# Performance work log

Measured on AMD Instinct MI355X. Metric: run time of the kernel, lower is better.

Reference implementation:

```python
import jax, jax.numpy as jnp
import numpy as np

B, T_PREV, T_CUR = 256, 128, 129
N_COV, N_TREAT, N_CONF = 30, 57, 5
H, FC = 128, 128
D_IN = N_COV + N_TREAT            # 87, lstm external input size
D_CELL = D_IN + N_CONF            # 92, cell input = [x_t, z_{t-1}]


def setup_inputs() -> dict:
    key = jax.random.key(0)
    ks = jax.random.split(key, 18)
    s = 0.05
    return {
        "previous_covariates": jax.random.normal(ks[0], (B, T_PREV, N_COV), jnp.float32),
        "previous_treatments": jax.random.normal(ks[1], (B, T_PREV, N_TREAT), jnp.float32),
        "current_covariates": jax.random.normal(ks[2], (B, T_CUR, N_COV), jnp.float32),
        "init_input": jax.random.normal(ks[3], (1, 1, D_IN), jnp.float32) * s,
        "h0": jax.random.normal(ks[4], (1, H), jnp.float32) * s,
        "c0": jax.random.normal(ks[5], (1, H), jnp.float32) * s,
        "z0": jax.random.normal(ks[6], (1, N_CONF), jnp.float32) * s,
        "W_ih": jax.random.normal(ks[7], (4 * H, D_CELL), jnp.float32) * s,
        "W_hh": jax.random.normal(ks[8], (4 * H, H), jnp.float32) * s,
        "b_ih": jax.random.normal(ks[9], (4 * H,), jnp.float32) * s,
        "b_hh": jax.random.normal(ks[10], (4 * H,), jnp.float32) * s,
        "W_z": jax.random.normal(ks[11], (N_CONF, H), jnp.float32) * s,
        "b_z": jax.random.normal(ks[12], (N_CONF,), jnp.float32) * s,
        "dec_W1": jax.random.normal(ks[13], (N_TREAT, N_COV + N_CONF, FC), jnp.float32) * s,
        "dec_b1": jax.random.normal(ks[14], (N_TREAT, FC), jnp.float32) * s,
        "dec_W2": jax.random.normal(ks[15], (N_TREAT, FC), jnp.float32) * s,
        "dec_b2": jax.random.normal(ks[16], (N_TREAT,), jnp.float32) * s,
    }


def _forward(previous_covariates, previous_treatments, current_covariates,
             init_input, h0, c0, z0, W_ih, W_hh, b_ih, b_hh, W_z, b_z,
             dec_W1, dec_b1, dec_W2, dec_b2):
    Bn = previous_covariates.shape[0]
    # (T_PREV, B, D_IN)
    x = jnp.concatenate([previous_covariates, previous_treatments], -1).transpose(1, 0, 2)
    # prepend trainable init input -> (T_CUR, B, D_IN)
    rnn_in = jnp.concatenate([jnp.broadcast_to(init_input, (1, Bn, D_IN)), x], 0)

    bias = b_ih + b_hh

    def step(carry, xt):
        h, c, z = carry
        inp = jnp.concatenate([xt, z], -1)                 # (B, D_CELL)
        gates = inp @ W_ih.T + h @ W_hh.T + bias           # (B, 4H)
        i, f, g, o = jnp.split(gates, 4, axis=-1)          # torch LSTMCell gate order
        c = jax.nn.sigmoid(f) * c + jax.nn.sigmoid(i) * jnp.tanh(g)
        h = jax.nn.sigmoid(o) * jnp.tanh(c)
        z = h @ W_z.T + b_z                                # (B, N_CONF)
        return (h, c, z), z

    carry0 = (jnp.broadcast_to(h0, (Bn, H)),
              jnp.broadcast_to(c0, (Bn, H)),
              jnp.broadcast_to(z0, (Bn, N_CONF)))
    _, zs = jax.lax.scan(step, carry0, rnn_in)             # (T_CUR, B, N_CONF)

    hidden_confounders = zs.reshape(-1, N_CONF)            # (T_CUR*B, N_CONF)
    covariates = current_covariates.transpose(1, 0, 2).reshape(-1, N_COV)
    # shapes match by construction (T_CUR*B rows each) -> no pad branch
    multitask_input = jnp.concatenate([hidden_confounders, covariates], -1)  # (N, 35)

    # batched per-treatment Linear -> LeakyReLU(0.01) -> Linear
    hdec = jax.nn.leaky_relu(
        jnp.einsum('nc,tcf->ntf', multitask_input, dec_W1) + dec_b1, 0.01)
    preds = jnp.einsum('ntf,tf->nt', hdec, dec_W2) + dec_b2                   # (N, 57)

    # T_CUR*B % (T_PREV) == 0 with these shapes -> no element trim
    confounders = hidden_confounders.reshape(T_PREV, -1, N_CONF)              # (128, 258, 5)
    return preds, confounders


def reference(previous_covariates, previous_treatments, current_covariates,
              init_input, h0, c0, z0, W_ih, W_hh, b_ih, b_hh, W_z, b_z,
              dec_W1, dec_b1, dec_W2, dec_b2):
    return _forward(previous_covariates, previous_treatments, current_covariates,
                    init_input, h0, c0, z0, W_ih, W_hh, b_ih, b_hh, W_z, b_z,
                    dec_W1, dec_b1, dec_W2, dec_b2)
```

## Files before the change

### kernel.cpp

```cpp
#include <hip/hip_runtime.h>
#include <stdint.h>

#define BATCH 256
#define T_PREVN 128
#define T_CURN 129
#define N_COV 30
#define N_TREAT 57
#define N_CONF 5
#define HID 128
#define D_IN 87
#define D_CELL 92
#define GATES 512
#define PRED_N (T_CURN*BATCH)
#define CONF_OFF (PRED_N*N_TREAT)

#define OFF_W1   0
#define SZ_W1    (57*8*2*64*8*2)
#define OFF_WIH  SZ_W1
#define SZ_WIH   (32*3*64*8*2)
#define OFF_GX   (OFF_W1 + SZ_W1 + SZ_WIH)
#define SZ_GX    (PRED_N*512*2)
#define OFF_MT   (OFF_GX + SZ_GX)
#define SZ_MT    (PRED_N*40*2)
#define WS_GX    (OFF_MT + SZ_MT)
#define WS_NEED  SZ_W1
#define WS_NEED2 (SZ_W1 + SZ_MT)

typedef _Float16 h2 __attribute__((ext_vector_type(2)));
typedef _Float16 h4 __attribute__((ext_vector_type(4)));
typedef _Float16 h8 __attribute__((ext_vector_type(8)));
typedef float f32x4 __attribute__((ext_vector_type(4)));

__device__ inline float rcp_fast(float x){
#if __has_builtin(__builtin_amdgcn_rcpf)
    return __builtin_amdgcn_rcpf(x);
#else
    return 1.0f / x;
#endif
}
__device__ inline float sigmoid_f(float x){ return rcp_fast(1.0f + __expf(-x)); }
__device__ inline float tanh_f(float x){ return 1.0f - 2.0f*rcp_fast(1.0f + __expf(2.0f*x)); }

__device__ inline float dot2f(h2 a, h2 b, float c){
#if __has_builtin(__builtin_amdgcn_fdot2)
    return __builtin_amdgcn_fdot2(a, b, c, false);
#else
    return c + (float)a.x*(float)b.x + (float)a.y*(float)b.y;
#endif
}
__device__ inline unsigned short f2us(float v){
    _Float16 h = (_Float16)v;
    return __builtin_bit_cast(unsigned short, h);
}
__device__ inline h2 us2h2(unsigned int u){
    return __builtin_bit_cast(h2, u);
}

__global__ __launch_bounds__(256) void prepack_wih(const float* __restrict__ W_ih,
                                                   _Float16* __restrict__ wihf)
{
    const int tid = blockIdx.x*256 + threadIdx.x;
    const int ct  = tid / 192;
    const int rem = tid - ct*192;
    const int ks  = rem >> 6;
    const int l   = rem & 63;
    const int gate = ct*16 + (l & 15);
    const int kb   = ks*32 + ((l >> 4) << 3);
    h8 v;
    #pragma unroll
    for (int j = 0; j < 8; j++){
        const int k = kb + j;
        v[j] = (k < D_IN) ? (_Float16)W_ih[gate*D_CELL + k] : (_Float16)0.0f;
    }
    *(h8*)(wihf + (size_t)tid*8) = v;
}

__global__ __launch_bounds__(256, 2) void gx_gemm(
    const float* __restrict__ pc, const float* __restrict__ pt,
    const float* __restrict__ init_input,
    const _Float16* __restrict__ wihf, _Float16* __restrict__ Gx)
{
    __shared__ alignas(16) _Float16 a_lds[64*104];
    __shared__ alignas(16) _Float16 gx_lds[64*264];

    const int tid = threadIdx.x;
    const int nb  = blockIdx.x * 64;

    for (int idx = tid; idx < 64*96; idx += 256){
        const int r = idx / 96;
        const int k = idx - r*96;
        const int n = nb + r;
        const int bb = n / 129;
        const int t  = n - bb*129;
        float v = 0.0f;
        if (k < D_IN){
            if (t == 0) v = init_input[k];
            else        v = (k < N_COV) ? pc[(bb*T_PREVN + t-1)*N_COV + k]
                                        : pt[(bb*T_PREVN + t-1)*N_TREAT + (k - N_COV)];
        }
        a_lds[r*104 + k] = (_Float16)v;
    }
    __syncthreads();

    const int w    = tid >> 6;
    const int l    = tid & 63;
    const int col  = l & 15;
    const int quad = l >> 4;

    const _Float16* ar = a_lds + (w*16 + col)*104 + quad*8;
    const h8 a0 = *(const h8*)(ar);
    const h8 a1 = *(const h8*)(ar + 32);
    const h8 a2 = *(const h8*)(ar + 64);

    for (int half = 0; half < 2; half++){
        #pragma unroll
        for (int ct8 = 0; ct8 < 16; ct8++){
            const int ct = half*16 + ct8;
            const _Float16* bp = wihf + (size_t)ct*1536 + l*8;
            const h8 b0 = *(const h8*)(bp);
            const h8 b1 = *(const h8*)(bp + 512);
            const h8 b2 = *(const h8*)(bp + 1024);
            f32x4 acc = {0.f, 0.f, 0.f, 0.f};
            acc = __builtin_amdgcn_mfma_f32_16x16x32_f16(a0, b0, acc, 0, 0, 0);
            acc = __builtin_amdgcn_mfma_f32_16x16x32_f16(a1, b1, acc, 0, 0, 0);
            acc = __builtin_amdgcn_mfma_f32_16x16x32_f16(a2, b2, acc, 0, 0, 0);
            #pragma unroll
            for (int r4 = 0; r4 < 4; r4++)
                gx_lds[(w*16 + quad*4 + r4)*264 + ct8*16 + col] = (_Float16)acc[r4];
        }
        __syncthreads();
        #pragma unroll
        for (int it = 0; it < 8; it++){
            const int idx = it*256 + tid;
            const int r   = idx >> 5;
            const int seg = idx & 31;
            *(h8*)(Gx + ((size_t)(nb + r))*512 + half*256 + seg*8) =
                *(const h8*)(&gx_lds[r*264 + seg*8]);
        }
        __syncthreads();
    }
}

__global__ __launch_bounds__(1024, 4) void lstm_scan_gx(
    const float* __restrict__ h0, const float* __restrict__ c0,
    const float* __restrict__ z0,
    const float* __restrict__ W_ih, const float* __restrict__ W_hh,
    const float* __restrict__ b_ih, const float* __restrict__ b_hh,
    const float* __restrict__ W_z, const float* __restrict__ b_z,
    const _Float16* __restrict__ Gx,
    float* __restrict__ zs_out, _Float16* __restrict__ mT)
{
    const int b   = blockIdx.x;
    const int tid = threadIdx.x;
    const int grp = tid >> 2;
    const int j   = tid & 3;
    const int g0  = grp*2, g1 = g0 + 1;

    __shared__ alignas(16) unsigned short v16h[128];
    __shared__ alignas(16) unsigned short hall[T_CURN*136];
    __shared__ alignas(16) float gbuf[GATES];
    __shared__ alignas(16) unsigned short gxc[2][16*512];
    __shared__ alignas(16) _Float16 wz16[5*HID];
    __shared__ alignas(16) float wzf[5*HID];
    __shared__ float z0c[5];

    for (int i = tid; i < 5*HID; i += 1024) wzf[i] = W_z[i];

    float c = 0.0f;
    if (tid < HID){ v16h[tid] = f2us(h0[tid]); c = c0[tid]; }

    if (tid < 5){
        float acc0 = 0.0f, acc1 = 0.0f;
        #pragma unroll 8
        for (int u = 0; u < HID; u += 2){
            acc0 += W_z[tid*HID + u]     * h0[u];
            acc1 += W_z[tid*HID + u + 1] * h0[u + 1];
        }
        z0c[tid] = z0[tid] - b_z[tid] - (acc0 + acc1);
    }
    {
        const int row = tid >> 6;
        const uint4 q = *(const uint4*)(Gx + ((size_t)b*T_CURN + row)*512 + (size_t)(tid & 63)*8);
        *(uint4*)(&gxc[0][tid*8]) = q;
    }
    __syncthreads();

    float wz0[5], wz1[5];
    #pragma unroll
    for (int z = 0; z < 5; z++){
        wz0[z] = W_ih[g0*D_CELL + D_IN + z];
        wz1[z] = W_ih[g1*D_CELL + D_IN + z];
    }
    float be0 = b_ih[g0] + b_hh[g0];
    float be1 = b_ih[g1] + b_hh[g1];
    #pragma unroll
    for (int z = 0; z < 5; z++){ be0 += wz0[z]*b_z[z]; be1 += wz1[z]*b_z[z]; }

    h2 w0[16], w1[16];
    {
        const int kb = j*32;
        #pragma unroll
        for (int i = 0; i < 16; i++){
            const int k = kb + 2*i;
            float f00 = W_hh[g0*HID + k],     f01 = W_hh[g0*HID + k + 1];
            float f10 = W_hh[g1*HID + k],     f11 = W_hh[g1*HID + k + 1];
            #pragma unroll
            for (int z = 0; z < 5; z++){
                const float a = wzf[z*HID + k], bb2 = wzf[z*HID + k + 1];
                f00 += wz0[z]*a;  f01 += wz0[z]*bb2;
                f10 += wz1[z]*a;  f11 += wz1[z]*bb2;
            }
            h2 p0; p0.x = (_Float16)f00; p0.y = (_Float16)f01; w0[i] = p0;
            h2 p1; p1.x = (_Float16)f10; p1.y = (_Float16)f11; w1[i] = p1;
        }
    }
    float b00 = be0, b01 = be1;
    #pragma unroll
    for (int z = 0; z < 5; z++){ b00 += wz0[z]*z0c[z]; b01 += wz1[z]*z0c[z]; }

    const unsigned short* vb = v16h + j*32;
    for (int t = 0; t < T_CURN; t++){
        const int cb = (t >> 4) & 1;
        uint4 pre;
        bool pok = false;
        if ((t & 15) == 0){
            const int row = t + 16 + (tid >> 6);
            pok = (row < T_CURN);
            if (pok)
                pre = *(const uint4*)(Gx + ((size_t)b*T_CURN + row)*512 + (size_t)(tid & 63)*8);
        }

        float s0a=0.f, s0b=0.f, s1a=0.f, s1b=0.f;
        #pragma unroll
        for (int i = 0; i < 4; i++){
            const uint4 q = *(const uint4*)(vb + i*8);
            s0a = dot2f(w0[4*i+0], us2h2(q.x), s0a);
            s0b = dot2f(w0[4*i+1], us2h2(q.y), s0b);
            s0a = dot2f(w0[4*i+2], us2h2(q.z), s0a);
            s0b = dot2f(w0[4*i+3], us2h2(q.w), s0b);
            s1a = dot2f(w1[4*i+0], us2h2(q.x), s1a);
            s1b = dot2f(w1[4*i+1], us2h2(q.y), s1b);
            s1a = dot2f(w1[4*i+2], us2h2(q.z), s1a);
            s1b = dot2f(w1[4*i+3], us2h2(q.w), s1b);
        }
        float s0 = s0a + s0b, s1 = s1a + s1b;
        s0 += __shfl_xor(s0, 1);  s0 += __shfl_xor(s0, 2);
        s1 += __shfl_xor(s1, 1);  s1 += __shfl_xor(s1, 2);
        if (j == 0){
            const h2 gx = us2h2(*(const unsigned int*)(&gxc[cb][(t & 15)*512 + g0]));
            float2 gg;
            gg.x = s0 + (float)gx.x + ((t == 0) ? b00 : be0);
            gg.y = s1 + (float)gx.y + ((t == 0) ? b01 : be1);
            *(float2*)(&gbuf[g0]) = gg;
        }
        __syncthreads();

        if (tid < HID){
            const float gi = gbuf[tid];
            const float gf = gbuf[128 + tid];
            const float gg = gbuf[256 + tid];
            const float go = gbuf[384 + tid];
            c = sigmoid_f(gf)*c + sigmoid_f(gi)*tanh_f(gg);
            const float h = sigmoid_f(go)*tanh_f(c);
            const unsigned short hu = f2us(h);
            v16h[tid] = hu;
            hall[t*136 + tid] = hu;
        }
        if (pok) *(uint4*)(&gxc[cb ^ 1][tid*8]) = pre;
        __syncthreads();
    }

    for (int i = tid; i < 5*HID; i += 1024) wz16[i] = (_Float16)W_z[i];
    __syncthreads();

    if (tid < T_CURN*N_CONF){
        const int t  = tid / 5;
        const int zi = tid - t*5;
        const uint4* hr = (const uint4*)(hall + t*136);
        const uint4* wr = (const uint4*)(wz16 + zi*HID);
        float a0 = 0.f, a1 = 0.f;
        #pragma unroll
        for (int i = 0; i < 16; i++){
            const uint4 hq = hr[i];
            const uint4 wq = wr[i];
            a0 = dot2f(us2h2(hq.x), us2h2(wq.x), a0);
            a1 = dot2f(us2h2(hq.y), us2h2(wq.y), a1);
            a0 = dot2f(us2h2(hq.z), us2h2(wq.z), a0);
            a1 = dot2f(us2h2(hq.w), us2h2(wq.w), a1);
        }
        const float z = a0 + a1 + b_z[zi];
        const int n = t*BATCH + b;
        zs_out[(size_t)n*N_CONF + zi] = z;
        if (mT) mT[(size_t)n*40 + zi] = (_Float16)z;
    }
}

__global__ __launch_bounds__(1024, 4) void lstm_scan_old(
    const float* __restrict__ pc, const float* __restrict__ pt,
    const float* __restrict__ init_input, const float* __restrict__ h0,
    const float* __restrict__ c0, const float* __restrict__ z0,
    const float* __restrict__ W_ih, const float* __restrict__ W_hh,
    const float* __restrict__ b_ih, const float* __restrict__ b_hh,
    const float* __restrict__ W_z, const float* __restrict__ b_z,
    float* __restrict__ zs_out, _Float16* __restrict__ mT)
{
    const int b   = blockIdx.x;
    const int tid = threadIdx.x;
    const int g   = tid >> 1;
    const int hf  = tid & 1;

    __shared__ alignas(16) unsigned short v16[224];
    __shared__ alignas(16) unsigned short xall[T_CURN*88];
    __shared__ alignas(16) unsigned short hall[T_CURN*136];
    __shared__ alignas(16) float gbuf[GATES];
    __shared__ alignas(16) _Float16 wz16[5*HID];
    __shared__ float z0c[5];

    float wzg[5];
    #pragma unroll
    for (int z = 0; z < 5; z++) wzg[z] = W_ih[g*D_CELL + 87 + z];

    float be = b_ih[g] + b_hh[g];
    #pragma unroll
    for (int z = 0; z < 5; z++) be += wzg[z] * b_z[z];

    h2 w[56];
    if (hf == 0){
        #pragma unroll
        for (int i = 0; i < 43; i++){
            h2 p; p.x = (_Float16)W_ih[g*D_CELL + 2*i];
                  p.y = (_Float16)W_ih[g*D_CELL + 2*i + 1];
            w[i] = p;
        }
        { h2 p; p.x = (_Float16)W_ih[g*D_CELL + 86]; p.y = (_Float16)0.0f; w[43] = p; }
        #pragma unroll
        for (int i = 44; i < 56; i++){
            const int u = 2*(i - 44);
            float f0 = W_hh[g*HID + u], f1 = W_hh[g*HID + u + 1];
            #pragma unroll
            for (int z = 0; z < 5; z++){
                f0 += wzg[z]*W_z[z*HID + u];
                f1 += wzg[z]*W_z[z*HID + u + 1];
            }
            h2 p; p.x = (_Float16)f0; p.y = (_Float16)f1;
            w[i] = p;
        }
    } else {
        #pragma unroll
        for (int i = 0; i < 52; i++){
            const int u = 24 + 2*i;
            float f0 = W_hh[g*HID + u], f1 = W_hh[g*HID + u + 1];
            #pragma unroll
            for (int z = 0; z < 5; z++){
                f0 += wzg[z]*W_z[z*HID + u];
                f1 += wzg[z]*W_z[z*HID + u + 1];
            }
            h2 p; p.x = (_Float16)f0; p.y = (_Float16)f1;
            w[i] = p;
        }
        #pragma unroll
        for (int i = 52; i < 56; i++){ h2 p; p.x=(_Float16)0.f; p.y=(_Float16)0.f; w[i]=p; }
    }

    for (int idx = tid; idx < T_CURN*88; idx += 1024){
        const int row = idx / 88;
        const int col = idx - row*88;
        float v = 0.0f;
        if (col < D_IN){
            if (row == 0) v = init_input[col];
            else {
                const int tp = row - 1;
                v = (col < N_COV) ? pc[(b*T_PREVN + tp)*N_COV + col]
                                  : pt[(b*T_PREVN + tp)*N_TREAT + (col - N_COV)];
            }
        }
        xall[idx] = f2us(v);
    }

    float c = 0.0f;
    if (tid < HID){ v16[88 + tid] = f2us(h0[tid]); c = c0[tid]; }
    if (tid >= 216 && tid < 224) v16[tid] = 0;

    if (tid < 5){
        float acc0 = 0.0f, acc1 = 0.0f;
        #pragma unroll 8
        for (int u = 0; u < HID; u += 2){
            acc0 += W_z[tid*HID + u]     * h0[u];
            acc1 += W_z[tid*HID + u + 1] * h0[u + 1];
        }
        z0c[tid] = z0[tid] - b_z[tid] - (acc0 + acc1);
    }
    __syncthreads();

    if (tid >= 128 && tid < 216) v16[tid - 128] = xall[tid - 128];
    float b0 = be;
    #pragma unroll
    for (int z = 0; z < 5; z++) b0 += wzg[z] * z0c[z];
    __syncthreads();

    const unsigned short* vbase = v16 + hf*112;
    for (int t = 0; t < T_CURN; t++){
        float a0 = 0.f, a1 = 0.f, a2 = 0.f, a3 = 0.f;
        #pragma unroll
        for (int i = 0; i < 14; i++){
            const uint4 q = *(const uint4*)(vbase + i*8);
            a0 = dot2f(w[4*i+0], us2h2(q.x), a0);
            a1 = dot2f(w[4*i+1], us2h2(q.y), a1);
            a2 = dot2f(w[4*i+2], us2h2(q.z), a2);
            a3 = dot2f(w[4*i+3], us2h2(q.w), a3);
        }
        float s = (a0 + a1) + (a2 + a3);
        s += __shfl_xor(s, 1);
        if (hf == 0) gbuf[g] = s + ((t == 0) ? b0 : be);
        __syncthreads();

        if (tid < HID){
            const float gi = gbuf[tid];
            const float gf = gbuf[128 + tid];
            const float gg = gbuf[256 + tid];
            const float go = gbuf[384 + tid];
            c = sigmoid_f(gf)*c + sigmoid_f(gi)*tanh_f(gg);
            const float h = sigmoid_f(go)*tanh_f(c);
            const unsigned short hu = f2us(h);
            v16[88 + tid] = hu;
            hall[t*136 + tid] = hu;
        } else if (tid < 216){
            if (t < T_PREVN) v16[tid - 128] = xall[(t + 1)*88 + (tid - 128)];
        }
        __syncthreads();
    }

    for (int i = tid; i < 5*HID; i += 1024) wz16[i] = (_Float16)W_z[i];
    __syncthreads();

    if (tid < T_CURN*N_CONF){
        const int t  = tid / 5;
        const int zi = tid - t*5;
        const uint4* hr = (const uint4*)(hall + t*136);
        const uint4* wr = (const uint4*)(wz16 + zi*HID);
        float a0 = 0.f, a1 = 0.f;
        #pragma unroll
        for (int i = 0; i < 16; i++){
            const uint4 hq = hr[i];
            const uint4 wq = wr[i];
            a0 = dot2f(us2h2(hq.x), us2h2(wq.x), a0);
            a1 = dot2f(us2h2(hq.y), us2h2(wq.y), a1);
            a0 = dot2f(us2h2(hq.z), us2h2(wq.z), a0);
            a1 = dot2f(us2h2(hq.w), us2h2(wq.w), a1);
        }
        const float z = a0 + a1 + b_z[zi];
        const int n = t*BATCH + b;
        zs_out[(size_t)n*N_CONF + zi] = z;
        if (mT) mT[(size_t)n*40 + zi] = (_Float16)z;
    }
}

__global__ __launch_bounds__(256) void prepack_w1(const float* __restrict__ dW1,
                                                  _Float16* __restrict__ wsh)
{
    const int tid = blockIdx.x*256 + threadIdx.x;
    const int treat = tid >> 10;
    const int r     = tid & 1023;
    const int ft    = r >> 7;
    const int ks    = (r >> 6) & 1;
    const int l     = r & 63;
    const int col   = ft*16 + (l & 15);
    const int kb    = ks*32 + ((l >> 4) << 3);
    h8 v;
    #pragma unroll
    for (int j = 0; j < 8; j++){
        const int k = kb + j;
        v[j] = (k < 35) ? (_Float16)dW1[(treat*35 + k)*128 + col] : (_Float16)0.0f;
    }
    *(h8*)(wsh + (size_t)tid*8) = v;
}

__global__ __launch_bounds__(256) void mt_cov(const float* __restrict__ cc,
                                              _Float16* __restrict__ mT)
{
    const int idx = blockIdx.x*256 + threadIdx.x;
    const int n   = idx / 5;
    const int oct = idx - n*5;
    const int b = n & 255;
    const int t = n >> 8;
    const float* crow = cc + ((size_t)b*T_CURN + t)*N_COV;
    h8 v;
    #pragma unroll
    for (int j = 0; j < 8; j++){
        const int cj = oct*8 + j;
        v[j] = (cj >= 5 && cj < 35) ? (_Float16)crow[cj - 5] : (_Float16)0.0f;
    }
    *(h8*)(mT + (size_t)n*40 + oct*8) = v;
}

__global__ __launch_bounds__(256, 2) void decoder_treat(
    const _Float16* __restrict__ mT, const _Float16* __restrict__ wsh,
    const float* __restrict__ db1, const float* __restrict__ dW2,
    const float* __restrict__ db2, float* __restrict__ preds)
{
    const int treat = blockIdx.x;
    const int rg    = blockIdx.y;
    const int w     = threadIdx.x >> 6;
    const int l     = threadIdx.x & 63;
    const int q     = l >> 4;
    const int r16   = l & 15;

    h8 bf0[8], bf1[8];
    const _Float16* bp = wsh + (size_t)treat*8192 + l*8;
    #pragma unroll
    for (int ft = 0; ft < 8; ft++){
        bf0[ft] = *(const h8*)(bp + ft*1024);
        bf1[ft] = *(const h8*)(bp + ft*1024 + 512);
    }
    float b1r[8], w2r[8], w2c[8];
    #pragma unroll
    for (int ft = 0; ft < 8; ft++){
        b1r[ft] = db1[treat*128 + ft*16 + r16];
        w2r[ft] = dW2[treat*128 + ft*16 + r16];
        w2c[ft] = 0.01f * w2r[ft];
    }
    const float b2 = db2[treat];

    const int tend = (rg + 1)*258;
    for (int tile = rg*258 + w; tile < tend; tile += 4){
        const int n = tile*16 + r16;
        const _Float16* mrow = mT + (size_t)n*40;
        const h8 a0 = *(const h8*)(mrow + q*8);
        h8 a1 = {};
        if (q == 0){
            const h4 t4 = *(const h4*)(mrow + 32);
            a1[0] = t4[0]; a1[1] = t4[1]; a1[2] = t4[2]; a1[3] = t4[3];
        }

        f32x4 pred = {0.f, 0.f, 0.f, 0.f};
        #pragma unroll
        for (int ft = 0; ft < 8; ft++){
            f32x4 acc = {b1r[ft], b1r[ft], b1r[ft], b1r[ft]};
            acc = __builtin_amdgcn_mfma_f32_16x16x32_f16(a0, bf0[ft], acc, 0, 0, 0);
            acc = __builtin_amdgcn_mfma_f32_16x16x32_f16(a1, bf1[ft], acc, 0, 0, 0);
            #pragma unroll
            for (int r = 0; r < 4; r++){
                const float a  = acc[r];
                const float mx = fmaxf(a, 0.0f);
                const float mn = fminf(a, 0.0f);
                pred[r] += mx*w2r[ft] + mn*w2c[ft];
            }
        }
        #pragma unroll
        for (int r = 0; r < 4; r++){
            float s = pred[r];
            s += __shfl_xor(s, 1);
            s += __shfl_xor(s, 2);
            s += __shfl_xor(s, 4);
            s += __shfl_xor(s, 8);
            pred[r] = s;
        }
        if (r16 == 0){
            #pragma unroll
            for (int r = 0; r < 4; r++)
                preds[(size_t)(tile*16 + q*4 + r)*N_TREAT + treat] = pred[r] + b2;
        }
    }
}

__global__ __launch_bounds__(256) void decoder_mfma(
    const float* __restrict__ cc, const float* __restrict__ zs,
    const _Float16* __restrict__ wsh,
    const float* __restrict__ db1, const float* __restrict__ dW2,
    const float* __restrict__ db2, float* __restrict__ preds)
{
    __shared__ alignas(16) _Float16 m_lds[64*72];

    const int tid  = threadIdx.x;
    const int base = blockIdx.x * 64;
    const int t    = base >> 8;

    for (int idx = tid; idx < 64*72; idx += 256){
        const int r = idx / 72;
        const int j = idx - r*72;
        const int n = base + r;
        const int b = n & 255;
        float v = 0.0f;
        if (j < 5)       v = zs[n*N_CONF + j];
        else if (j < 35) v = cc[(b*T_CURN + t)*N_COV + (j - 5)];
        m_lds[r*72 + j] = (_Float16)v;
    }
    __syncthreads();

    const int w    = tid >> 6;
    const int l    = tid & 63;
    const int row  = l & 15;
    const int quad = l >> 4;

    const _Float16* arow = m_lds + (w*16 + row)*72 + quad*8;
    const h8 a0 = *(const h8*)(arow);
    const h8 a1 = *(const h8*)(arow + 32);
    const int nbase = base + w*16 + quad*4;

    for (int treat = 0; treat < 57; treat++){
        const _Float16* bp = wsh + (size_t)treat*8192 + l*8;
        f32x4 pred = {0.0f, 0.0f, 0.0f, 0.0f};
        #pragma unroll
        for (int ft = 0; ft < 8; ft++){
            const h8 b0 = *(const h8*)(bp + ft*1024);
            const h8 b1 = *(const h8*)(bp + ft*1024 + 512);
            f32x4 acc = {0.0f, 0.0f, 0.0f, 0.0f};
            acc = __builtin_amdgcn_mfma_f32_16x16x32_f16(a0, b0, acc, 0, 0, 0);
            acc = __builtin_amdgcn_mfma_f32_16x16x32_f16(a1, b1, acc, 0, 0, 0);
            const int col = ft*16 + row;
            const float hb1 = db1[treat*128 + col];
            const float hw2 = dW2[treat*128 + col];
            #pragma unroll
            for (int r = 0; r < 4; r++){
                float hd = acc[r] + hb1;
                hd = (hd > 0.0f) ? hd : 0.01f*hd;
                pred[r] += hd * hw2;
            }
        }
        #pragma unroll
        for (int r = 0; r < 4; r++){
            float s = pred[r];
            s += __shfl_xor(s, 1);
            s += __shfl_xor(s, 2);
            s += __shfl_xor(s, 4);
            s += __shfl_xor(s, 8);
            pred[r] = s;
        }
        if (row == 0){
            const float b2 = db2[treat];
            #pragma unroll
            for (int r = 0; r < 4; r++)
                preds[(size_t)(nbase + r)*N_TREAT + treat] = pred[r] + b2;
        }
    }
}

__global__ __launch_bounds__(256) void decoder_fallback(
    const float* __restrict__ cc, const float* __restrict__ zs,
    const float* __restrict__ dW1, const float* __restrict__ db1,
    const float* __restrict__ dW2, const float* __restrict__ db2,
    float* __restrict__ preds)
{
    const int t     = blockIdx.x;
    const int treat = blockIdx.y;
    const int tid   = threadIdx.x;

    __shared__ alignas(16) float w1t[128*36];
    __shared__ float b1s[128];
    __shared__ float w2s[128];

    for (int it = tid; it < 35*128; it += 256){
        const int cidx = it >> 7;
        const int f    = it & 127;
        w1t[f*36 + cidx] = dW1[(treat*35 + cidx)*128 + f];
    }
    if (tid < 128){
        b1s[tid] = db1[treat*128 + tid];
        w2s[tid] = dW2[treat*128 + tid];
        w1t[tid*36 + 35] = 0.0f;
    }
    __syncthreads();

    const int n = t*BATCH + tid;
    float m[36];
    #pragma unroll
    for (int j = 0; j < N_CONF; j++) m[j] = zs[n*N_CONF + j];
    #pragma unroll
    for (int j = 0; j < N_COV; j++)  m[N_CONF + j] = cc[(tid*T_CURN + t)*N_COV + j];
    m[35] = 0.0f;

    const float b2 = db2[treat];
    float pred = 0.0f;
    for (int f = 0; f < 128; f++){
        float a = b1s[f];
        const float4* wr = (const float4*)(w1t + f*36);
        #pragma unroll
        for (int cq = 0; cq < 9; cq++){
            const float4 v = wr[cq];
            a += m[cq*4+0]*v.x + m[cq*4+1]*v.y + m[cq*4+2]*v.z + m[cq*4+3]*v.w;
        }
        a = (a > 0.0f) ? a : 0.01f*a;
        pred += a * w2s[f];
    }
    preds[n*N_TREAT + treat] = pred + b2;
}

extern "C" void kernel_launch(void* const* d_in, const int* in_sizes, int n_in,
                              void* d_out, int out_size, void* d_ws, size_t ws_size,
                              hipStream_t stream)
{
    const float* pc   = (const float*)d_in[0];
    const float* pt   = (const float*)d_in[1];
    const float* cc   = (const float*)d_in[2];
    const float* init = (const float*)d_in[3];
    const float* h0   = (const float*)d_in[4];
    const float* c0   = (const float*)d_in[5];
    const float* z0   = (const float*)d_in[6];
    const float* W_ih = (const float*)d_in[7];
    const float* W_hh = (const float*)d_in[8];
    const float* b_ih = (const float*)d_in[9];
    const float* b_hh = (const float*)d_in[10];
    const float* W_z  = (const float*)d_in[11];
    const float* b_z  = (const float*)d_in[12];
    const float* dW1  = (const float*)d_in[13];
    const float* db1  = (const float*)d_in[14];
    const float* dW2  = (const float*)d_in[15];
    const float* db2  = (const float*)d_in[16];

    float* preds = (float*)d_out;
    float* zs    = (float*)d_out + CONF_OFF;

    if (ws_size >= (size_t)WS_GX){
        _Float16* wsh  = (_Float16*)d_ws;
        _Float16* wihf = (_Float16*)((char*)d_ws + OFF_WIH);
        _Float16* Gx   = (_Float16*)((char*)d_ws + OFF_GX);
        _Float16* mT   = (_Float16*)((char*)d_ws + OFF_MT);

        prepack_w1<<<228, 256, 0, stream>>>(dW1, wsh);
        prepack_wih<<<24, 256, 0, stream>>>(W_ih, wihf);
        mt_cov<<<645, 256, 0, stream>>>(cc, mT);
        gx_gemm<<<516, 256, 0, stream>>>(pc, pt, init, wihf, Gx);
        lstm_scan_gx<<<BATCH, 1024, 0, stream>>>(h0, c0, z0, W_ih, W_hh,
                                                 b_ih, b_hh, W_z, b_z, Gx, zs, mT);
        decoder_treat<<<dim3(N_TREAT, 8), 256, 0, stream>>>(mT, wsh, db1, dW2, db2, preds);
    } else if (ws_size >= (size_t)WS_NEED2){
        _Float16* wsh = (_Float16*)d_ws;
        _Float16* mT  = (_Float16*)((char*)d_ws + WS_NEED);
        prepack_w1<<<228, 256, 0, stream>>>(dW1, wsh);
        mt_cov<<<645, 256, 0, stream>>>(cc, mT);
        lstm_scan_old<<<BATCH, 1024, 0, stream>>>(pc, pt, init, h0, c0, z0,
                                                  W_ih, W_hh, b_ih, b_hh, W_z, b_z, zs, mT);
        decoder_treat<<<dim3(N_TREAT, 8), 256, 0, stream>>>(mT, wsh, db1, dW2, db2, preds);
    } else if (ws_size >= (size_t)WS_NEED){
        _Float16* wsh = (_Float16*)d_ws;
        prepack_w1<<<228, 256, 0, stream>>>(dW1, wsh);
        lstm_scan_old<<<BATCH, 1024, 0, stream>>>(pc, pt, init, h0, c0, z0,
                                                  W_ih, W_hh, b_ih, b_hh, W_z, b_z,
                                                  zs, (_Float16*)nullptr);
        decoder_mfma<<<516, 256, 0, stream>>>(cc, zs, wsh, db1, dW2, db2, preds);
    } else {
        lstm_scan_old<<<BATCH, 1024, 0, stream>>>(pc, pt, init, h0, c0, z0,
                                                  W_ih, W_hh, b_ih, b_hh, W_z, b_z,
                                                  zs, (_Float16*)nullptr);
        decoder_fallback<<<dim3(T_CURN, N_TREAT), 256, 0, stream>>>(
            cc, zs, dW1, db1, dW2, db2, preds);
    }
}
```

Before: 228.3 us.

## Fuse per-treatment decoder into LSTM scan tail and merge weight prepack kernels

Each scan block now builds its [z, covariates] activation tile in shared memory and runs the per-treatment MFMA decoder itself. This removes the separate mt_cov and decoder_treat launches and the global mT round trip. The two weight-prepack kernels are merged into one launch, and the hidden-state vector is double-buffered by timestep parity. In exchange, every scan block reloads all decoder weights from L2, and the decoder runs on only 256 blocks instead of a separate wider grid. A leftover single-iteration loop before the real scan adds a little redundant work.

```diff
diff --git a/kernel.cpp b/kernel.cpp
--- a/kernel.cpp
+++ b/kernel.cpp
@@ -56,23 +56,43 @@
     return __builtin_bit_cast(h2, u);
 }
 
-__global__ __launch_bounds__(256) void prepack_wih(const float* __restrict__ W_ih,
-                                                   _Float16* __restrict__ wihf)
+__global__ __launch_bounds__(256) void prep_w1wih(
+    const float* __restrict__ dW1, const float* __restrict__ W_ih,
+    _Float16* __restrict__ wsh, _Float16* __restrict__ wihf)
 {
-    const int tid = blockIdx.x*256 + threadIdx.x;
-    const int ct  = tid / 192;
-    const int rem = tid - ct*192;
-    const int ks  = rem >> 6;
-    const int l   = rem & 63;
-    const int gate = ct*16 + (l & 15);
-    const int kb   = ks*32 + ((l >> 4) << 3);
-    h8 v;
-    #pragma unroll
-    for (int j = 0; j < 8; j++){
-        const int k = kb + j;
-        v[j] = (k < D_IN) ? (_Float16)W_ih[gate*D_CELL + k] : (_Float16)0.0f;
-    }
-    *(h8*)(wihf + (size_t)tid*8) = v;
+    const int bid = blockIdx.x;
+    if (bid < 228){
+        const int tid = bid*256 + threadIdx.x;
+        const int treat = tid >> 10;
+        const int r     = tid & 1023;
+        const int ft    = r >> 7;
+        const int ks    = (r >> 6) & 1;
+        const int l     = r & 63;
+        const int col   = ft*16 + (l & 15);
+        const int kb    = ks*32 + ((l >> 4) << 3);
+        h8 v;
+        #pragma unroll
+        for (int j = 0; j < 8; j++){
+            const int k = kb + j;
+            v[j] = (k < 35) ? (_Float16)dW1[(treat*35 + k)*128 + col] : (_Float16)0.0f;
+        }
+        *(h8*)(wsh + (size_t)tid*8) = v;
+    } else {
+        const int tid = (bid - 228)*256 + threadIdx.x;
+        const int ct  = tid / 192;
+        const int rem = tid - ct*192;
+        const int ks  = rem >> 6;
+        const int l   = rem & 63;
+        const int gate = ct*16 + (l & 15);
+        const int kb   = ks*32 + ((l >> 4) << 3);
+        h8 v;
+        #pragma unroll
+        for (int j = 0; j < 8; j++){
+            const int k = kb + j;
+            v[j] = (k < D_IN) ? (_Float16)W_ih[gate*D_CELL + k] : (_Float16)0.0f;
+        }
+        *(h8*)(wihf + (size_t)tid*8) = v;
+    }
 }
 
 __global__ __launch_bounds__(256, 2) void gx_gemm(
@@ -141,14 +161,16 @@
     }
 }
 
-__global__ __launch_bounds__(1024, 4) void lstm_scan_gx(
+__global__ __launch_bounds__(1024, 4) void lstm_scan_fused(
     const float* __restrict__ h0, const float* __restrict__ c0,
     const float* __restrict__ z0,
     const float* __restrict__ W_ih, const float* __restrict__ W_hh,
     const float* __restrict__ b_ih, const float* __restrict__ b_hh,
     const float* __restrict__ W_z, const float* __restrict__ b_z,
-    const _Float16* __restrict__ Gx,
-    float* __restrict__ zs_out, _Float16* __restrict__ mT)
+    const _Float16* __restrict__ Gx, const float* __restrict__ cc,
+    const _Float16* __restrict__ wsh, const float* __restrict__ db1,
+    const float* __restrict__ dW2, const float* __restrict__ db2,
+    float* __restrict__ zs_out, float* __restrict__ preds)
 {
     const int b   = blockIdx.x;
     const int tid = threadIdx.x;
@@ -156,32 +178,33 @@
     const int j   = tid & 3;
     const int g0  = grp*2, g1 = g0 + 1;
 
-    __shared__ alignas(16) unsigned short v16h[128];
+    __shared__ alignas(16) unsigned short v16h[128 + 128];
     __shared__ alignas(16) unsigned short hall[T_CURN*136];
-    __shared__ alignas(16) float gbuf[GATES];
     __shared__ alignas(16) unsigned short gxc[2][16*512];
+    __shared__ alignas(16) float wzf[5*HID];
     __shared__ alignas(16) _Float16 wz16[5*HID];
-    __shared__ alignas(16) float wzf[5*HID];
+    __shared__ alignas(16) _Float16 m_lds[144*40];
     __shared__ float z0c[5];
 
-    for (int i = tid; i < 5*HID; i += 1024) wzf[i] = W_z[i];
-
-    float c = 0.0f;
-    if (tid < HID){ v16h[tid] = f2us(h0[tid]); c = c0[tid]; }
-
+    for (int i = tid; i < 5*HID; i += 1024){
+        const float v = W_z[i];
+        wzf[i]  = v;
+        wz16[i] = (_Float16)v;
+    }
+    if (tid < HID) v16h[tid] = f2us(h0[tid]);
     if (tid < 5){
         float acc0 = 0.0f, acc1 = 0.0f;
         #pragma unroll 8
-        for (int u = 0; u < HID; u += 2){
-            acc0 += W_z[tid*HID + u]     * h0[u];
-            acc1 += W_z[tid*HID + u + 1] * h0[u + 1];
+        for (int k = 0; k < HID; k += 2){
+            acc0 += W_z[tid*HID + k]     * h0[k];
+            acc1 += W_z[tid*HID + k + 1] * h0[k + 1];
         }
         z0c[tid] = z0[tid] - b_z[tid] - (acc0 + acc1);
     }
     {
         const int row = tid >> 6;
-        const uint4 q = *(const uint4*)(Gx + ((size_t)b*T_CURN + row)*512 + (size_t)(tid & 63)*8);
-        *(uint4*)(&gxc[0][tid*8]) = q;
+        const uint4 p = *(const uint4*)(Gx + ((size_t)b*T_CURN + row)*512 + (size_t)(tid & 63)*8);
+        *(uint4*)(&gxc[0][(row << 9) + (tid & 63)*8]) = p;
     }
     __syncthreads();
 
@@ -218,9 +241,11 @@
     #pragma unroll
     for (int z = 0; z < 5; z++){ b00 += wz0[z]*z0c[z]; b01 += wz1[z]*z0c[z]; }
 
-    const unsigned short* vb = v16h + j*32;
+    __shared__ alignas(16) float gbuf[GATES];
+    const unsigned short* vb0 = v16h + j*32;
     for (int t = 0; t < T_CURN; t++){
         const int cb = (t >> 4) & 1;
+        const unsigned short* vb = vb0 + (t & 1)*128;
         uint4 pre;
         bool pok = false;
         if ((t & 15) == 0){
@@ -260,39 +285,205 @@
             const float gf = gbuf[128 + tid];
             const float gg = gbuf[256 + tid];
             const float go = gbuf[384 + tid];
-            c = sigmoid_f(gf)*c + sigmoid_f(gi)*tanh_f(gg);
-            const float h = sigmoid_f(go)*tanh_f(c);
-            const unsigned short hu = f2us(h);
-            v16h[tid] = hu;
-            hall[t*136 + tid] = hu;
-        }
+            float c = (t == 0) ? c0[tid]
+                               : __builtin_bit_cast(float, *(const unsigned int*)(&gbuf[0]) ) ;
+            (void)c;
+        }
+        __syncthreads();
         if (pok) *(uint4*)(&gxc[cb ^ 1][tid*8]) = pre;
-        __syncthreads();
-    }
-
-    for (int i = tid; i < 5*HID; i += 1024) wz16[i] = (_Float16)W_z[i];
-    __syncthreads();
+        if (false) {}
+        break;
+    }
+
+    {
+        float c = (tid < HID) ? c0[tid] : 0.0f;
+        for (int t = 0; t < T_CURN; t++){
+            const int cb = (t >> 4) & 1;
+            const unsigned short* vb = vb0 + (t & 1)*128;
+            uint4 pre;
+            bool pok = false;
+            if ((t & 15) == 0){
+                const int row = t + 16 + (tid >> 6);
+                pok = (row < T_CURN);
+                if (pok)
+                    pre = *(const uint4*)(Gx + ((size_t)b*T_CURN + row)*512 + (size_t)(tid & 63)*8);
+            }
+
+            float s0a=0.f, s0b=0.f, s1a=0.f, s1b=0.f;
+            #pragma unroll
+            for (int i = 0; i < 4; i++){
+                const uint4 q = *(const uint4*)(vb + i*8);
+                s0a = dot2f(w0[4*i+0], us2h2(q.x), s0a);
+                s0b = dot2f(w0[4*i+1], us2h2(q.y), s0b);
+                s0a = dot2f(w0[4*i+2], us2h2(q.z), s0a);
+                s0b = dot2f(w0[4*i+3], us2h2(q.w), s0b);
+                s1a = dot2f(w1[4*i+0], us2h2(q.x), s1a);
+                s1b = dot2f(w1[4*i+1], us2h2(q.y), s1b);
+                s1a = dot2f(w1[4*i+2], us2h2(q.z), s1a);
+                s1b = dot2f(w1[4*i+3], us2h2(q.w), s1b);
+            }
+            float s0 = s0a + s0b, s1 = s1a + s1b;
+            s0 += __shfl_xor(s0, 1);  s0 += __shfl_xor(s0, 2);
+            s1 += __shfl_xor(s1, 1);  s1 += __shfl_xor(s1, 2);
+            if (j == 0){
+                const h2 gx = us2h2(*(const unsigned int*)(&gxc[cb][(t & 15)*512 + g0]));
+                float2 gg;
+                gg.x = s0 + (float)gx.x + ((t == 0) ? b00 : be0);
+                gg.y = s1 + (float)gx.y + ((t == 0) ? b01 : be1);
+                *(float2*)(&gbuf[g0]) = gg;
+            }
+            __syncthreads();
+
+            if (tid < HID){
+                const float gi = gbuf[tid];
+                const float gf = gbuf[128 + tid];
+                const float gg = gbuf[256 + tid];
+                const float go = gbuf[384 + tid];
+                c = sigmoid_f(gf)*c + sigmoid_f(gi)*tanh_f(gg);
+                const float h = sigmoid_f(go)*tanh_f(c);
+                const unsigned short hu = f2us(h);
+                v16h[((t + 1) & 1)*128 + tid] = hu;
+                hall[t*136 + tid] = hu;
+            }
+            if (pok) *(uint4*)(&gxc[cb ^ 1][tid*8]) = pre;
+            __syncthreads();
+        }
+    }
 
     if (tid < T_CURN*N_CONF){
         const int t  = tid / 5;
         const int zi = tid - t*5;
         const uint4* hr = (const uint4*)(hall + t*136);
         const uint4* wr = (const uint4*)(wz16 + zi*HID);
-        float a0 = 0.f, a1 = 0.f;
+        float s0 = 0.f, s1 = 0.f;
         #pragma unroll
         for (int i = 0; i < 16; i++){
             const uint4 hq = hr[i];
             const uint4 wq = wr[i];
-            a0 = dot2f(us2h2(hq.x), us2h2(wq.x), a0);
-            a1 = dot2f(us2h2(hq.y), us2h2(wq.y), a1);
-            a0 = dot2f(us2h2(hq.z), us2h2(wq.z), a0);
-            a1 = dot2f(us2h2(hq.w), us2h2(wq.w), a1);
-        }
-        const float z = a0 + a1 + b_z[zi];
-        const int n = t*BATCH + b;
-        zs_out[(size_t)n*N_CONF + zi] = z;
-        if (mT) mT[(size_t)n*40 + zi] = (_Float16)z;
-    }
+            s0 = dot2f(us2h2(hq.x), us2h2(wq.x), s0);
+            s1 = dot2f(us2h2(hq.y), us2h2(wq.y), s1);
+            s0 = dot2f(us2h2(hq.z), us2h2(wq.z), s0);
+            s1 = dot2f(us2h2(hq.w), us2h2(wq.w), s1);
+        }
+        const float z = s0 + s1 + b_z[zi];
+        zs_out[(size_t)(t*BATCH + b)*N_CONF + zi] = z;
+        m_lds[t*40 + zi] = (_Float16)z;
+    }
+    for (int idx = tid; idx < 144*40; idx += 1024){
+        const int t   = idx / 40;
+        const int cjj = idx - t*40;
+        if (cjj < 5) continue;
+        float v = 0.0f;
+        if (t < T_CURN && cjj < 35)
+            v = cc[((size_t)b*T_CURN + t)*N_COV + (cjj - 5)];
+        m_lds[idx] = (_Float16)v;
+    }
+    __syncthreads();
+
+    {
+        const int wv  = tid >> 6;
+        const int l   = tid & 63;
+        const int q   = l >> 4;
+        const int r16 = l & 15;
+
+        for (int treat = wv; treat < N_TREAT; treat += 16){
+            h8 bf0[8], bf1[8];
+            const _Float16* bp = wsh + (size_t)treat*8192 + l*8;
+            #pragma unroll
+            for (int ft = 0; ft < 8; ft++){
+                bf0[ft] = *(const h8*)(bp + ft*1024);
+                bf1[ft] = *(const h8*)(bp + ft*1024 + 512);
+            }
+            float b1r[8], w2r[8], w2c[8];
+            #pragma unroll
+            for (int ft = 0; ft < 8; ft++){
+                b1r[ft] = db1[treat*128 + ft*16 + r16];
+                w2r[ft] = dW2[treat*128 + ft*16 + r16];
+                w2c[ft] = 0.01f * w2r[ft];
+            }
+            const float b2 = db2[treat];
+
+            for (int tile = 0; tile < 9; tile++){
+                const _Float16* mrow = m_lds + (tile*16 + r16)*40;
+                const h8 a0 = *(const h8*)(mrow + q*8);
+                h8 a1 = {};
+                if (q == 0){
+                    const h4 t4 = *(const h4*)(mrow + 32);
+                    a1[0] = t4[0]; a1[1] = t4[1]; a1[2] = t4[2]; a1[3] = t4[3];
+                }
+
+                f32x4 pred = {0.f, 0.f, 0.f, 0.f};
+                #pragma unroll
+                for (int ft = 0; ft < 8; ft++){
+                    f32x4 acc = {b1r[ft], b1r[ft], b1r[ft], b1r[ft]};
+                    acc = __builtin_amdgcn_mfma_f32_16x16x32_f16(a0, bf0[ft], acc, 0, 0, 0);
+                    acc = __builtin_amdgcn_mfma_f32_16x16x32_f16(a1, bf1[ft], acc, 0, 0, 0);
+                    #pragma unroll
+                    for (int r = 0; r < 4; r++){
+                        const float a  = acc[r];
+                        const float mx = fmaxf(a, 0.0f);
+                        const float mn = fminf(a, 0.0f);
+                        pred[r] += mx*w2r[ft] + mn*w2c[ft];
+                    }
+                }
+                #pragma unroll
+                for (int r = 0; r < 4; r++){
+                    float s = pred[r];
+                    s += __shfl_xor(s, 1);
+                    s += __shfl_xor(s, 2);
+                    s += __shfl_xor(s, 4);
+                    s += __shfl_xor(s, 8);
+                    pred[r] = s;
+                }
+                if (r16 == 0){
+                    #pragma unroll
+                    for (int r = 0; r < 4; r++){
+                        const int t = tile*16 + q*4 + r;
+                        if (t < T_CURN)
+                            preds[((size_t)t*BATCH + b)*N_TREAT + treat] = pred[r] + b2;
+                    }
+                }
+            }
+        }
+    }
+}
+
+__global__ __launch_bounds__(256) void prepack_w1(const float* __restrict__ dW1,
+                                                  _Float16* __restrict__ wsh)
+{
+    const int tid = blockIdx.x*256 + threadIdx.x;
+    const int treat = tid >> 10;
+    const int r     = tid & 1023;
+    const int ft    = r >> 7;
+    const int ks    = (r >> 6) & 1;
+    const int l     = r & 63;
+    const int col   = ft*16 + (l & 15);
+    const int kb    = ks*32 + ((l >> 4) << 3);
+    h8 v;
+    #pragma unroll
+    for (int j = 0; j < 8; j++){
+        const int k = kb + j;
+        v[j] = (k < 35) ? (_Float16)dW1[(treat*35 + k)*128 + col] : (_Float16)0.0f;
+    }
+    *(h8*)(wsh + (size_t)tid*8) = v;
+}
+
+__global__ __launch_bounds__(256) void mt_cov(const float* __restrict__ cc,
+                                              _Float16* __restrict__ mT)
+{
+    const int idx = blockIdx.x*256 + threadIdx.x;
+    const int n   = idx / 5;
+    const int oct = idx - n*5;
+    const int b = n & 255;
+    const int t = n >> 8;
+    const float* crow = cc + ((size_t)b*T_CURN + t)*N_COV;
+    h8 v;
+    #pragma unroll
+    for (int j = 0; j < 8; j++){
+        const int cj = oct*8 + j;
+        v[j] = (cj >= 5 && cj < 35) ? (_Float16)crow[cj - 5] : (_Float16)0.0f;
+    }
+    *(h8*)(mT + (size_t)n*40 + oct*8) = v;
 }
 
 __global__ __launch_bounds__(1024, 4) void lstm_scan_old(
@@ -455,44 +646,6 @@
     }
 }
 
-__global__ __launch_bounds__(256) void prepack_w1(const float* __restrict__ dW1,
-                                                  _Float16* __restrict__ wsh)
-{
-    const int tid = blockIdx.x*256 + threadIdx.x;
-    const int treat = tid >> 10;
-    const int r     = tid & 1023;
-    const int ft    = r >> 7;
-    const int ks    = (r >> 6) & 1;
-    const int l     = r & 63;
-    const int col   = ft*16 + (l & 15);
-    const int kb    = ks*32 + ((l >> 4) << 3);
-    h8 v;
-    #pragma unroll
-    for (int j = 0; j < 8; j++){
-        const int k = kb + j;
-        v[j] = (k < 35) ? (_Float16)dW1[(treat*35 + k)*128 + col] : (_Float16)0.0f;
-    }
-    *(h8*)(wsh + (size_t)tid*8) = v;
-}
-
-__global__ __launch_bounds__(256) void mt_cov(const float* __restrict__ cc,
-                                              _Float16* __restrict__ mT)
-{
-    const int idx = blockIdx.x*256 + threadIdx.x;
-    const int n   = idx / 5;
-    const int oct = idx - n*5;
-    const int b = n & 255;
-    const int t = n >> 8;
-    const float* crow = cc + ((size_t)b*T_CURN + t)*N_COV;
-    h8 v;
-    #pragma unroll
-    for (int j = 0; j < 8; j++){
-        const int cj = oct*8 + j;
-        v[j] = (cj >= 5 && cj < 35) ? (_Float16)crow[cj - 5] : (_Float16)0.0f;
-    }
-    *(h8*)(mT + (size_t)n*40 + oct*8) = v;
-}
-
 __global__ __launch_bounds__(256, 2) void decoder_treat(
     const _Float16* __restrict__ mT, const _Float16* __restrict__ wsh,
     const float* __restrict__ db1, const float* __restrict__ dW2,
@@ -559,78 +712,6 @@
             #pragma unroll
             for (int r = 0; r < 4; r++)
                 preds[(size_t)(tile*16 + q*4 + r)*N_TREAT + treat] = pred[r] + b2;
-        }
-    }
-}
-
-__global__ __launch_bounds__(256) void decoder_mfma(
-    const float* __restrict__ cc, const float* __restrict__ zs,
-    const _Float16* __restrict__ wsh,
-    const float* __restrict__ db1, const float* __restrict__ dW2,
-    const float* __restrict__ db2, float* __restrict__ preds)
-{
-    __shared__ alignas(16) _Float16 m_lds[64*72];
-
-    const int tid  = threadIdx.x;
-    const int base = blockIdx.x * 64;
-    const int t    = base >> 8;
-
-    for (int idx = tid; idx < 64*72; idx += 256){
-        const int r = idx / 72;
-        const int j = idx - r*72;
-        const int n = base + r;
-        const int b = n & 255;
-        float v = 0.0f;
-        if (j < 5)       v = zs[n*N_CONF + j];
-        else if (j < 35) v = cc[(b*T_CURN + t)*N_COV + (j - 5)];
-        m_lds[r*72 + j] = (_Float16)v;
-    }
-    __syncthreads();
-
-    const int w    = tid >> 6;
-    const int l    = tid & 63;
-    const int row  = l & 15;
-    const int quad = l >> 4;
-
-    const _Float16* arow = m_lds + (w*16 + row)*72 + quad*8;
-    const h8 a0 = *(const h8*)(arow);
-    const h8 a1 = *(const h8*)(arow + 32);
-    const int nbase = base + w*16 + quad*4;
-
-    for (int treat = 0; treat < 57; treat++){
-        const _Float16* bp = wsh + (size_t)treat*8192 + l*8;
-        f32x4 pred = {0.0f, 0.0f, 0.0f, 0.0f};
-        #pragma unroll
-        for (int ft = 0; ft < 8; ft++){
-            const h8 b0 = *(const h8*)(bp + ft*1024);
-            const h8 b1 = *(const h8*)(bp + ft*1024 + 512);
-            f32x4 acc = {0.0f, 0.0f, 0.0f, 0.0f};
-            acc = __builtin_amdgcn_mfma_f32_16x16x32_f16(a0, b0, acc, 0, 0, 0);
-            acc = __builtin_amdgcn_mfma_f32_16x16x32_f16(a1, b1, acc, 0, 0, 0);
-            const int col = ft*16 + row;
-            const float hb1 = db1[treat*128 + col];
-            const float hw2 = dW2[treat*128 + col];
-            #pragma unroll
-            for (int r = 0; r < 4; r++){
-                float hd = acc[r] + hb1;
-                hd = (hd > 0.0f) ? hd : 0.01f*hd;
-                pred[r] += hd * hw2;
-            }
-        }
-        #pragma unroll
-        for (int r = 0; r < 4; r++){
-            float s = pred[r];
-            s += __shfl_xor(s, 1);
-            s += __shfl_xor(s, 2);
-            s += __shfl_xor(s, 4);
-            s += __shfl_xor(s, 8);
-            pred[r] = s;
-        }
-        if (row == 0){
-            const float b2 = db2[treat];
-            #pragma unroll
-            for (int r = 0; r < 4; r++)
-                preds[(size_t)(nbase + r)*N_TREAT + treat] = pred[r] + b2;
         }
     }
 }
@@ -714,15 +795,12 @@
         _Float16* wsh  = (_Float16*)d_ws;
         _Float16* wihf = (_Float16*)((char*)d_ws + OFF_WIH);
         _Float16* Gx   = (_Float16*)((char*)d_ws + OFF_GX);
-        _Float16* mT   = (_Float16*)((char*)d_ws + OFF_MT);
-
-        prepack_w1<<<228, 256, 0, stream>>>(dW1, wsh);
-        prepack_wih<<<24, 256, 0, stream>>>(W_ih, wihf);
-        mt_cov<<<645, 256, 0, stream>>>(cc, mT);
+
+        prep_w1wih<<<252, 256, 0, stream>>>(dW1, W_ih, wsh, wihf);
         gx_gemm<<<516, 256, 0, stream>>>(pc, pt, init, wihf, Gx);
-        lstm_scan_gx<<<BATCH, 1024, 0, stream>>>(h0, c0, z0, W_ih, W_hh,
-                                                 b_ih, b_hh, W_z, b_z, Gx, zs, mT);
-        decoder_treat<<<dim3(N_TREAT, 8), 256, 0, stream>>>(mT, wsh, db1, dW2, db2, preds);
+        lstm_scan_fused<<<BATCH, 1024, 0, stream>>>(h0, c0, z0, W_ih, W_hh,
+                                                    b_ih, b_hh, W_z, b_z, Gx, cc,
+                                                    wsh, db1, dW2, db2, zs, preds);
     } else if (ws_size >= (size_t)WS_NEED2){
         _Float16* wsh = (_Float16*)d_ws;
         _Float16* mT  = (_Float16*)((char*)d_ws + WS_NEED);
@@ -731,13 +809,6 @@
         lstm_scan_old<<<BATCH, 1024, 0, stream>>>(pc, pt, init, h0, c0, z0,
                                                   W_ih, W_hh, b_ih, b_hh, W_z, b_z, zs, mT);
         decoder_treat<<<dim3(N_TREAT, 8), 256, 0, stream>>>(mT, wsh, db1, dW2, db2, preds);
-    } else if (ws_size >= (size_t)WS_NEED){
-        _Float16* wsh = (_Float16*)d_ws;
-        prepack_w1<<<228, 256, 0, stream>>>(dW1, wsh);
-        lstm_scan_old<<<BATCH, 1024, 0, stream>>>(pc, pt, init, h0, c0, z0,
-                                                  W_ih, W_hh, b_ih, b_hh, W_z, b_z,
-                                                  zs, (_Float16*)nullptr);
-        decoder_mfma<<<516, 256, 0, stream>>>(cc, zs, wsh, db1, dW2, db2, preds);
     } else {
         lstm_scan_old<<<BATCH, 1024, 0, stream>>>(pc, pt, init, h0, c0, z0,
                                                   W_ih, W_hh, b_ih, b_hh, W_z, b_z,
```

New measurement: 215.3 us. 5.7% less time.
